# Optimization experiments

Measured on AMD Instinct MI355X. Metric: run time of the kernel, lower is better.

The kernel has to match this reference:

```python
import jax, jax.numpy as jnp
import numpy as np

L = 4          # num layers
NH = 128       # hidden channels per layer
FC = 16        # frame_channel = patch^2 * C
HP = 32        # H / patch
WP = 32        # W / patch
K = 5          # filter_size
B = 8
T_PREV = 10
T_AFTER = 10
T_TOTAL = T_PREV + T_AFTER - 1  # 19 generated frames
FORGET_BIAS = 1.0


def _conv(x, w):
    # x: [B, Cin, H, W], w: [Cout, Cin, kh, kw], stride 1, SAME padding
    return jax.lax.conv_general_dilated(
        x, w, (1, 1), 'SAME', dimension_numbers=('NCHW', 'OIHW', 'NCHW'))


def _st_lstm_cell(x, h, c, m, Wx, Wh, Wm, Wo, Wl):
    # Standard PredRNN SpatioTemporalLSTMCell (bias-free convs, no layer norm)
    xc = _conv(x, Wx)   # [B, 7*NH, H, W]
    hc = _conv(h, Wh)   # [B, 4*NH, H, W]
    mc = _conv(m, Wm)   # [B, 3*NH, H, W]
    i_x, f_x, g_x, i_xp, f_xp, g_xp, o_x = jnp.split(xc, 7, axis=1)
    i_h, f_h, g_h, o_h = jnp.split(hc, 4, axis=1)
    i_m, f_m, g_m = jnp.split(mc, 3, axis=1)

    i_t = jax.nn.sigmoid(i_x + i_h)
    f_t = jax.nn.sigmoid(f_x + f_h + FORGET_BIAS)
    g_t = jnp.tanh(g_x + g_h)
    c_new = f_t * c + i_t * g_t

    i_tp = jax.nn.sigmoid(i_xp + i_m)
    f_tp = jax.nn.sigmoid(f_xp + f_m + FORGET_BIAS)
    g_tp = jnp.tanh(g_xp + g_m)
    m_new = f_tp * m + i_tp * g_tp

    mem = jnp.concatenate([c_new, m_new], axis=1)  # [B, 2*NH, H, W]
    o_t = jax.nn.sigmoid(o_x + o_h + _conv(mem, Wo))
    h_new = o_t * jnp.tanh(_conv(mem, Wl))
    return h_new, c_new, m_new


def setup_inputs() -> dict:
    key = jax.random.key(0)
    ks = jax.random.split(key, 9)
    s = jnp.float32(0.02)  # small init scale to keep gates in a sane range
    return {
        'frames_tensor': jax.random.normal(ks[0], (B, T_PREV + T_AFTER, HP, WP, FC), jnp.float32),
        'mask_true': jax.random.uniform(ks[1], (B, T_AFTER - 1, HP, WP, FC), jnp.float32),
        'Wx0': jax.random.normal(ks[2], (7 * NH, FC, K, K), jnp.float32) * s,
        'Wx': jax.random.normal(ks[3], (L - 1, 7 * NH, NH, K, K), jnp.float32) * s,
        'Wh': jax.random.normal(ks[4], (L, 4 * NH, NH, K, K), jnp.float32) * s,
        'Wm': jax.random.normal(ks[5], (L, 3 * NH, NH, K, K), jnp.float32) * s,
        'Wo': jax.random.normal(ks[6], (L, NH, 2 * NH, K, K), jnp.float32) * s,
        'Wl': jax.random.normal(ks[7], (L, NH, 2 * NH, 1, 1), jnp.float32) * s,
        'Wout': jax.random.normal(ks[8], (FC, NH, 1, 1), jnp.float32) * s,
    }


def reference(frames_tensor, mask_true, Wx0, Wx, Wh, Wm, Wo, Wl, Wout):
    # [B,T,H,W,C] -> [B,T,C,H,W]
    frames = jnp.transpose(frames_tensor, (0, 1, 4, 2, 3))
    mask = jnp.transpose(mask_true, (0, 1, 4, 2, 3))

    # For t < data_previous the input is the ground-truth frame (mask == 1);
    # afterwards it is blended with the previous generation x_gen.
    ones = jnp.ones((B, T_PREV, FC, HP, WP), frames.dtype)
    mask_seq = jnp.concatenate([ones, mask], axis=1)  # [B, T_TOTAL, C, H, W]

    frames_t = jnp.transpose(frames[:, :T_TOTAL], (1, 0, 2, 3, 4))  # [T,B,C,H,W]
    mask_t = jnp.transpose(mask_seq, (1, 0, 2, 3, 4))               # [T,B,C,H,W]

    h0 = jnp.zeros((L, B, NH, HP, WP), frames.dtype)
    c0 = jnp.zeros((L, B, NH, HP, WP), frames.dtype)
    m0 = jnp.zeros((B, NH, HP, WP), frames.dtype)
    xg0 = jnp.zeros((B, FC, HP, WP), frames.dtype)

    def step(carry, xs):
        h, c, m, x_gen = carry
        frame, msk = xs
        net = msk * frame + (1.0 - msk) * x_gen
        h_new, c_new, m = _st_lstm_cell(net, h[0], c[0], m, Wx0, Wh[0], Wm[0], Wo[0], Wl[0])
        hs, cs = [h_new], [c_new]
        for i in range(1, L):
            hi, ci, m = _st_lstm_cell(hs[-1], h[i], c[i], m, Wx[i - 1], Wh[i], Wm[i], Wo[i], Wl[i])
            hs.append(hi)
            cs.append(ci)
        x_gen = _conv(hs[-1], Wout)  # 1x1 conv, no bias
        return (jnp.stack(hs), jnp.stack(cs), m, x_gen), x_gen

    _, next_frames = jax.lax.scan(step, (h0, c0, m0, xg0), (frames_t, mask_t))
    # [T,B,C,H,W] -> [B,T,H,W,C]
    return jnp.transpose(next_frames, (1, 0, 3, 4, 2))
```

## Files before the change

kernel.cpp:

```cpp
#include <hip/hip_runtime.h>
#include <math.h>

#define TT 19
#define TPREV 10

typedef __attribute__((ext_vector_type(8))) short bf8v;
typedef __attribute__((ext_vector_type(4))) float f4v;
typedef __attribute__((ext_vector_type(16))) float f16v;

__device__ __forceinline__ float sigmoidf_(float x){ return 1.f/(1.f+expf(-x)); }
__device__ __forceinline__ unsigned short f2bf(float x){
    unsigned int u = __float_as_uint(x);
    u += 0x7FFFu + ((u>>16)&1u);
    return (unsigned short)(u>>16);
}
__device__ __forceinline__ float bf2f(unsigned short b){ return __uint_as_float(((unsigned int)b)<<16); }

#define GLDS(g, l) __builtin_amdgcn_global_load_lds( \
    (const __attribute__((address_space(1))) void*)(g),   \
    (__attribute__((address_space(3))) void*)(l), 16, 0, 0)

struct HSeg {
    const unsigned short* in;
    int cl;
    int c0;
    int nch;
    int tap0, ntaps, five;
};
struct HJob {
    const unsigned short* wt;
    float* out;
    int cout_stride, pad;
    HSeg s;
};
struct HJobs14 { HJob j[14]; };
struct HJobs9  { HJob j[9]; };


template<typename JOBS>
__global__ __launch_bounds__(256, 2) void hconvA_kernel(JOBS jobs)
{
    __shared__ unsigned short sA[16384];
    __shared__ unsigned short sH[15360];
    const int tid = threadIdx.x;

    const int nb   = gridDim.x * gridDim.y;
    const int per8 = nb >> 3;
    const int bidl = blockIdx.x + gridDim.x * blockIdx.y;
    const int g    = (bidl & 7) * per8 + (bidl >> 3);
    const int jy   = g >> 5;
    const int xt   = g & 31;
    const HJob jb = jobs.j[jy];

    const int ng0 = xt << 8;
    const int bb = ng0 >> 10, p0 = ng0 & 1023;
    const int y0 = p0 >> 5;

    const int lane = tid & 63, wv = tid >> 6;
    const int wm = (wv & 1) << 6;
    const int wn = (wv >> 1) << 7;
    const int col = lane & 31, ll5 = lane >> 5;

    int bofs0[4];
#pragma unroll
    for (int ni = 0; ni < 4; ++ni) {
        const int ln = wn + ni * 32 + col;
        const int cell = ((ln >> 5) + 2) * 40 + (ln & 31) + 4;
        bofs0[ni] = cell * 8 + ll5 * 3840;
    }
    const int rowA0 = (wm + col) * 8;
    const int oA = ll5 * 1024;

    f16v acc[2][4];
#pragma unroll
    for (int i = 0; i < 2; ++i)
#pragma unroll
        for (int j = 0; j < 4; ++j) acc[i][j] = (f16v)0.f;

    const HSeg sg = jb.s;
    const unsigned short* inb = sg.in + ((size_t)bb << (10 + sg.cl));
    const unsigned short* wptr = jb.wt;
    const int ntaps = sg.ntaps;
    const int ntot = sg.nch * ntaps;

    {
        const int c0 = sg.c0;
#pragma unroll
        for (int k = 0; k < 8; ++k) {
            const int s = tid + k * 256;
            if (s < 1920) {
                const int r = s / 160;
                const int rem = s - r * 160;
                const int cc = rem >> 2, G = rem & 3;
                const int y = y0 + r - 2, x = cc - 4;
                const bool okv = ((unsigned)y < 32u) & ((unsigned)x < 32u);
                const int yc = okv ? y : 0, xc = okv ? x : 0;
                bf8v v = *(const bf8v*)(inb + ((((yc << 5) + xc)) << sg.cl) + c0 + G * 8);
                if (!okv) v = (bf8v)(short)0;
                *(bf8v*)&sH[(G * 480 + r * 40 + cc) * 8] = v;
            }
        }
    }
    GLDS(wptr + tid * 8,                &sA[tid * 8]);
    GLDS(wptr + (tid + 256) * 8,        &sA[(tid + 256) * 8]);
    GLDS(wptr + 4096 + tid * 8,         &sA[4096 + tid * 8]);
    GLDS(wptr + 4096 + (tid + 256) * 8, &sA[4096 + (tid + 256) * 8]);
    wptr += 8192;

    int bcur = 0, tc = 0, ch = 0;
    for (int t = 0; t < ntot; ++t) {
        if (tc == ntaps) {
            tc = 0; ++ch;
            __syncthreads();
            const int c0 = sg.c0 + ch * 32;
#pragma unroll
            for (int k = 0; k < 8; ++k) {
                const int s = tid + k * 256;
                if (s < 1920) {
                    const int r = s / 160;
                    const int rem = s - r * 160;
                    const int cc = rem >> 2, G = rem & 3;
                    const int y = y0 + r - 2, x = cc - 4;
                    const bool okv = ((unsigned)y < 32u) & ((unsigned)x < 32u);
                    const int yc = okv ? y : 0, xc = okv ? x : 0;
                    bf8v v = *(const bf8v*)(inb + ((((yc << 5) + xc)) << sg.cl) + c0 + G * 8);
                    if (!okv) v = (bf8v)(short)0;
                    *(bf8v*)&sH[(G * 480 + r * 40 + cc) * 8] = v;
                }
            }
        }
        if (t + 2 < ntot) {
            const int b2 = (bcur + 2) & 3;
            GLDS(wptr + tid * 8,         &sA[b2 * 4096 + tid * 8]);
            GLDS(wptr + (tid + 256) * 8, &sA[b2 * 4096 + (tid + 256) * 8]);
            wptr += 4096;
        }
        int tO = 0;
        if (sg.five) {
            const int tap = sg.tap0 + tc;
            const int t5 = (tap * 52) >> 8;
            tO = ((t5 - 2) * 40 + (tap - t5 * 5 - 2)) * 8;
        }
        if (t + 2 < ntot)      asm volatile("s_waitcnt vmcnt(4) lgkmcnt(0)" ::: "memory");
        else if (t + 1 < ntot) asm volatile("s_waitcnt vmcnt(2) lgkmcnt(0)" ::: "memory");
        else                   asm volatile("s_waitcnt vmcnt(0) lgkmcnt(0)" ::: "memory");
        __builtin_amdgcn_s_barrier();
        __builtin_amdgcn_sched_barrier(0);

        const unsigned short* sAb = &sA[bcur * 4096];
        bf8v av[2][2], bv[2][4];
#pragma unroll
        for (int s = 0; s < 2; ++s) {
#pragma unroll
            for (int mi = 0; mi < 2; ++mi)
                av[s][mi] = *(const bf8v*)&sAb[s * 2048 + oA + rowA0 + mi * 256];
#pragma unroll
            for (int ni = 0; ni < 4; ++ni)
                bv[s][ni] = *(const bf8v*)&sH[bofs0[ni] + tO + s * 7680];
        }
        __builtin_amdgcn_s_setprio(1);
#pragma unroll
        for (int s = 0; s < 2; ++s)
#pragma unroll
            for (int mi = 0; mi < 2; ++mi)
#pragma unroll
                for (int ni = 0; ni < 4; ++ni)
                    acc[mi][ni] = __builtin_amdgcn_mfma_f32_32x32x16_bf16(
                        av[s][mi], bv[s][ni], acc[mi][ni], 0, 0, 0);
        __builtin_amdgcn_s_setprio(0);

        bcur = (bcur + 1) & 3;
        ++tc;
    }

    const int nfix = ng0 + wn + col;
#pragma unroll
    for (int ni = 0; ni < 4; ++ni) {
        const int n = nfix + ni * 32;
        float* ob = jb.out + (size_t)n * jb.cout_stride;
#pragma unroll
        for (int mi = 0; mi < 2; ++mi) {
            const int mb = wm + mi * 32 + 4 * ll5;
            const f16v a = acc[mi][ni];
#pragma unroll
            for (int qd = 0; qd < 4; ++qd) {
                f4v v;
                v[0] = a[qd * 4 + 0]; v[1] = a[qd * 4 + 1];
                v[2] = a[qd * 4 + 2]; v[3] = a[qd * 4 + 3];
                *(f4v*)(ob + mb + qd * 8) = v;
            }
        }
    }
}

template<typename JOBS>
__global__ __launch_bounds__(256) void hconv_kernel(JOBS jobs)
{
    __shared__ unsigned short sA[8192];
    __shared__ unsigned short sH[10240];
    const HJob jb = jobs.j[blockIdx.y];
    const int tid = threadIdx.x;

    const int ng0 = blockIdx.x * 128;
    const int bb = ng0 >> 10, p0 = ng0 & 1023;
    const int y0 = p0 >> 5;

    const int lane = tid & 63, wv = tid >> 6;
    const int wm = (wv & 1) << 6;
    const int wn = (wv >> 1) << 6;
    const int col = lane & 31, ll5 = lane >> 5;

    int bofs0[2];
#pragma unroll
    for (int ni = 0; ni < 2; ++ni) {
        const int ln = wn + ni * 32 + col;
        const int cell = ((ln >> 5) + 2) * 40 + (ln & 31) + 4;
        bofs0[ni] = cell * 8 + ll5 * 2560;
    }

    f16v acc[2][2];
#pragma unroll
    for (int i = 0; i < 2; ++i)
#pragma unroll
        for (int j = 0; j < 2; ++j) acc[i][j] = (f16v)0.f;

    const HSeg sg = jb.s;
    const unsigned short* inb = sg.in + ((size_t)bb << (10 + sg.cl));
    const unsigned short* wptr = jb.wt;
    int buf = 0;
    bool first = true;
    for (int ch = 0; ch < sg.nch; ++ch) {
        const int c0 = sg.c0 + ch * 32;
#pragma unroll
        for (int k = 0; k < 5; ++k) {
            const int s = tid + k * 256;
            const int r = s / 160;
            const int rem = s - r * 160;
            const int cc = rem >> 2, G = rem & 3;
            const int y = y0 + r - 2, x = cc - 4;
            const bool okv = ((unsigned)y < 32u) & ((unsigned)x < 32u);
            const int yc = okv ? y : 0, xc = okv ? x : 0;
            bf8v v = *(const bf8v*)(inb + ((((yc << 5) + xc)) << sg.cl) + c0 + G * 8);
            if (!okv) v = (bf8v)(short)0;
            *(bf8v*)&sH[(G * 320 + r * 40 + cc) * 8] = v;
        }
        if (first) {
            GLDS(wptr + tid * 8,         &sA[tid * 8]);
            GLDS(wptr + (tid + 256) * 8, &sA[(tid + 256) * 8]);
            wptr += 4096;
            first = false;
        }
        __syncthreads();
        for (int t = 0; t < sg.ntaps; ++t) {
            GLDS(wptr + tid * 8,         &sA[(buf ^ 1) * 4096 + tid * 8]);
            GLDS(wptr + (tid + 256) * 8, &sA[(buf ^ 1) * 4096 + (tid + 256) * 8]);
            wptr += 4096;
            int tO = 0;
            if (sg.five) {
                const int tap = sg.tap0 + t;
                const int t5 = (tap * 52) >> 8;
                tO = ((t5 - 2) * 40 + (tap - t5 * 5 - 2)) * 8;
            }
            const unsigned short* sAb = &sA[buf * 4096];
#pragma unroll
            for (int s = 0; s < 2; ++s) {
                const int o = s * 2 + ll5;
                bf8v av[2], bv[2];
#pragma unroll
                for (int mi = 0; mi < 2; ++mi)
                    av[mi] = *(const bf8v*)&sAb[(o * 128 + wm + mi * 32 + col) * 8];
#pragma unroll
                for (int ni = 0; ni < 2; ++ni)
                    bv[ni] = *(const bf8v*)&sH[bofs0[ni] + tO + s * 5120];
#pragma unroll
                for (int mi = 0; mi < 2; ++mi)
#pragma unroll
                    for (int ni = 0; ni < 2; ++ni)
                        acc[mi][ni] = __builtin_amdgcn_mfma_f32_32x32x16_bf16(
                            av[mi], bv[ni], acc[mi][ni], 0, 0, 0);
            }
            __syncthreads();
            buf ^= 1;
        }
    }

    const int nfix = ng0 + wn + col;
#pragma unroll
    for (int ni = 0; ni < 2; ++ni) {
        const int n = nfix + ni * 32;
        float* ob = jb.out + (size_t)n * jb.cout_stride;
#pragma unroll
        for (int mi = 0; mi < 2; ++mi) {
            const int mb = wm + mi * 32 + 4 * ll5;
            const f16v a = acc[mi][ni];
#pragma unroll
            for (int qd = 0; qd < 4; ++qd) {
                f4v v;
                v[0] = a[qd * 4 + 0]; v[1] = a[qd * 4 + 1];
                v[2] = a[qd * 4 + 2]; v[3] = a[qd * 4 + 3];
                *(f4v*)(ob + mb + qd * 8) = v;
            }
        }
    }
}

__global__ __launch_bounds__(256) void packT_kernel(
    const float* __restrict__ src, unsigned short* __restrict__ dst,
    int Cin, int srcTaps, int rowOff, int ci0, int ntaps, int tap0,
    int ciMax, int total)
{
    const int idx = blockIdx.x * 256 + threadIdx.x;
    if (idx >= total) return;
    const int j = idx & 7;
    const int row = (idx >> 3) & 127;
    const int q = (idx >> 10) & 3;
    const int at = idx >> 12;
    const int ch = at / ntaps;
    const int tap = tap0 + (at - ch * ntaps);
    const int ci = ci0 + ch * 32 + q * 8 + j;
    float v = 0.f;
    if (ci < ciMax)
        v = src[((size_t)(rowOff + row) * Cin + ci) * srcTaps + tap];
    dst[idx] = f2bf(v);
}

__global__ __launch_bounds__(256) void net_kernel(
    const float* __restrict__ frames, const float* __restrict__ mask,
    const float* __restrict__ xgen, unsigned short* __restrict__ net, int t)
{
    const int idx = blockIdx.x * 256 + threadIdx.x;
    const int n = idx >> 5, ch = idx & 31;
    float v = 0.f;
    if (ch < 16) {
        const int b = n >> 10, p = n & 1023;
        const float fr = frames[((((size_t)b * 20 + t) << 10) + p) * 16 + ch];
        if (t < TPREV) v = fr;
        else {
            const float mk = mask[((((size_t)b * 9 + (t - TPREV)) << 10) + p) * 16 + ch];
            v = mk * fr + (1.f - mk) * xgen[(size_t)n * 16 + ch];
        }
    }
    net[idx] = f2bf(v);
}

__global__ __launch_bounds__(256) void gates_kernel(
    const float* __restrict__ preA, const float* __restrict__ preB,
    float* __restrict__ c, float* __restrict__ m,
    unsigned short* __restrict__ m_bf, unsigned short* __restrict__ mem)
{
    const int idx = blockIdx.x * 256 + threadIdx.x;
    const int n = idx >> 7, ch = idx & 127;
    const float* pa = preA + (size_t)n * 896 + ch;
    const float* pb = preB + (size_t)n * 896 + ch;
    const float i_ = pa[0]   + pb[0];
    const float f_ = pa[128] + pb[128];
    const float g_ = pa[256] + pb[256];
    const float ip = pa[384] + pb[384];
    const float fp = pa[512] + pb[512];
    const float gp = pa[640] + pb[640];
    const float cn = sigmoidf_(f_ + 1.f) * c[idx] + sigmoidf_(i_) * tanhf(g_);
    const float mn = sigmoidf_(fp + 1.f) * m[idx] + sigmoidf_(ip) * tanhf(gp);
    c[idx] = cn;
    m[idx] = mn;
    m_bf[idx] = f2bf(mn);
    mem[(size_t)n * 256 + ch] = f2bf(cn);
    mem[(size_t)n * 256 + 128 + ch] = f2bf(mn);
}

__global__ __launch_bounds__(256) void hout_kernel(
    const float* __restrict__ preA, const float* __restrict__ preB,
    const float* __restrict__ opart, const float* __restrict__ lconv,
    unsigned short* __restrict__ h)
{
    const int idx = blockIdx.x * 256 + threadIdx.x;
    const int n = idx >> 7, ch = idx & 127;
    float oc = preA[(size_t)n * 896 + 768 + ch] + preB[(size_t)n * 896 + 768 + ch];
#pragma unroll
    for (int j = 0; j < 8; ++j) oc += opart[idx + (size_t)j * 1048576];
    h[idx] = f2bf(sigmoidf_(oc) * tanhf(lconv[idx]));
}

__global__ __launch_bounds__(256) void wout_kernel(
    const unsigned short* __restrict__ h3, const float* __restrict__ wo,
    float* __restrict__ xgen, float* __restrict__ out, int t)
{
    const int idx = blockIdx.x * 256 + threadIdx.x;
    const int n = idx >> 4, ch = idx & 15;
    const int b = n >> 10, p = n & 1023;
    const unsigned short* hr = h3 + (size_t)n * 128;
    const float* wr = wo + ch * 128;
    float acc = 0.f;
#pragma unroll 8
    for (int ci = 0; ci < 128; ++ci)
        acc = fmaf(bf2f(hr[ci]), wr[ci], acc);
    xgen[idx] = acc;
    out[((((size_t)b * TT + t) << 10) + p) * 16 + ch] = acc;
}

extern "C" void kernel_launch(void* const* d_in, const int* in_sizes, int n_in,
                              void* d_out, int out_size, void* d_ws, size_t ws_size,
                              hipStream_t stream)
{
    const float* frames = (const float*)d_in[0];
    const float* mask   = (const float*)d_in[1];
    const float* Wx0    = (const float*)d_in[2];
    const float* Wx     = (const float*)d_in[3];
    const float* Wh     = (const float*)d_in[4];
    const float* Wm     = (const float*)d_in[5];
    const float* Wo     = (const float*)d_in[6];
    const float* Wl     = (const float*)d_in[7];
    const float* Wout   = (const float*)d_in[8];
    float* out = (float*)d_out;

    char* base = (char*)d_ws;
    size_t off = 0;
    auto take = [&](size_t bytes) -> char* {
        char* p = base + off;
        off = (off + bytes + 255) & ~(size_t)255;
        return p;
    };
    float* c0            = (float*)take(4ull * 1048576 * 4);
    float* m32           = (float*)take((size_t)1048576 * 4);
    unsigned short* hbf  = (unsigned short*)take(4ull * 1048576 * 2);
    unsigned short* mbf  = (unsigned short*)take((size_t)1048576 * 2);
    const size_t zbytes = off;
    float* xgen          = (float*)take((size_t)131072 * 4);
    float* preA          = (float*)take((size_t)8192 * 896 * 4);
    float* preB          = (float*)take((size_t)8192 * 896 * 4);
    float* lconv         = (float*)take((size_t)1048576 * 4);
    float* opart         = (float*)take(8ull * 1048576 * 4);
    unsigned short* net  = (unsigned short*)take((size_t)262144 * 2);
    unsigned short* mem  = (unsigned short*)take((size_t)2097152 * 2);
    unsigned short* pa0xT = (unsigned short*)take(((size_t)7 * 25 * 4096 + 4096) * 2);
    unsigned short* paT0 = (unsigned short*)take(((size_t)7 * 100 * 4096 + 4096) * 2);
    unsigned short* paT1 = (unsigned short*)take(((size_t)7 * 200 * 4096 + 4096) * 2);
    unsigned short* paT2 = (unsigned short*)take(((size_t)7 * 200 * 4096 + 4096) * 2);
    unsigned short* paT3 = (unsigned short*)take(((size_t)7 * 200 * 4096 + 4096) * 2);
    unsigned short* paT[4] = { paT0, paT1, paT2, paT3 };
    unsigned short* oT   = (unsigned short*)take((4ull * 200 * 4096 + 4096) * 2);
    unsigned short* lT   = (unsigned short*)take((4ull * 8 * 4096 + 4096) * 2);

    hipMemsetAsync(d_ws, 0, zbytes, stream);

    auto packT = [&](const float* s, unsigned short* d, int Cin, int srcTaps,
                     int rowOff, int ci0, int nch, int ntaps, int tap0, int ciMax) {
        const int total = nch * ntaps * 4096;
        packT_kernel<<<(total + 255) / 256, 256, 0, stream>>>(
            s, d, Cin, srcTaps, rowOff, ci0, ntaps, tap0, ciMax, total);
    };
    const int CIMAXBIG = 1 << 30;
    for (int g = 0; g < 7; ++g) {
        packT(Wx0, pa0xT + (size_t)g * 25 * 4096, 16, 25, g * 128, 0, 1, 25, 0, 16);
        const float* hm0 = (g < 3) ? (Wh + (size_t)g * 128 * 128 * 25)
                         : (g == 6) ? (Wh + (size_t)384 * 128 * 25)
                                    : (Wm + (size_t)(g - 3) * 128 * 128 * 25);
        packT(hm0, paT0 + (size_t)g * 100 * 4096, 128, 25, 0, 0, 4, 25, 0, CIMAXBIG);
        for (int l = 1; l < 4; ++l) {
            packT(Wx + (size_t)(l - 1) * 896 * 128 * 25,
                  paT[l] + (size_t)g * 200 * 4096, 128, 25, g * 128, 0, 4, 25, 0, CIMAXBIG);
            const float* hmsrc = (g < 3) ? (Wh + ((size_t)l * 512 + g * 128) * 128 * 25)
                               : (g == 6) ? (Wh + ((size_t)l * 512 + 384) * 128 * 25)
                                          : (Wm + ((size_t)l * 384 + (g - 3) * 128) * 128 * 25);
            packT(hmsrc, paT[l] + ((size_t)g * 200 + 100) * 4096, 128, 25, 0, 0, 4, 25, 0, CIMAXBIG);
        }
    }
    for (int l = 0; l < 4; ++l) {
        packT(Wo + (size_t)l * 128 * 256 * 25, oT + (size_t)l * 200 * 4096,
              256, 25, 0, 0, 8, 25, 0, CIMAXBIG);
        packT(Wl + (size_t)l * 128 * 256, lT + (size_t)l * 8 * 4096,
              256, 1, 0, 0, 8, 1, 0, CIMAXBIG);
    }

    for (int t = 0; t < TT; ++t) {
        net_kernel<<<1024, 256, 0, stream>>>(frames, mask, xgen, net, t);
        for (int l = 0; l < 4; ++l) {
            unsigned short* hl = hbf + (size_t)l * 1048576;
            HJobs14 JA{};
            if (l == 0) {
                for (int g = 0; g < 7; ++g) {
                    const unsigned short* hmsrc = (g < 3 || g == 6) ? hl : mbf;
                    JA.j[2 * g] = HJob{ pa0xT + (size_t)g * 25 * 4096, preA + g * 128,
                                        896, 0, HSeg{ net, 5, 0, 1, 0, 25, 1 } };
                    JA.j[2 * g + 1] = HJob{ paT0 + (size_t)g * 100 * 4096, preB + g * 128,
                                            896, 0, HSeg{ hmsrc, 7, 0, 4, 0, 25, 1 } };
                }
            } else {
                for (int g = 0; g < 7; ++g) {
                    const unsigned short* hmsrc = (g < 3 || g == 6) ? hl : mbf;
                    JA.j[g] = HJob{ paT[l] + (size_t)g * 200 * 4096, preA + g * 128,
                                    896, 0, HSeg{ hbf + (size_t)(l - 1) * 1048576, 7, 0, 4, 0, 25, 1 } };
                    JA.j[7 + g] = HJob{ paT[l] + ((size_t)g * 200 + 100) * 4096, preB + g * 128,
                                        896, 0, HSeg{ hmsrc, 7, 0, 4, 0, 25, 1 } };
                }
            }
            hconvA_kernel<HJobs14><<<dim3(32, 14), 256, 0, stream>>>(JA);

            gates_kernel<<<4096, 256, 0, stream>>>(preA, preB,
                c0 + (size_t)l * 1048576, m32, mbf, mem);

            HJobs9 JB{};
            for (int jj = 0; jj < 8; ++jj)
                JB.j[jj] = HJob{ oT + ((size_t)l * 200 + jj * 25) * 4096,
                                 opart + (size_t)jj * 1048576, 128, 0,
                                 HSeg{ mem, 8, jj * 32, 1, 0, 25, 1 } };
            JB.j[8] = HJob{ lT + (size_t)l * 8 * 4096, lconv, 128, 0,
                            HSeg{ mem, 8, 0, 8, 0, 1, 0 } };
            hconv_kernel<HJobs9><<<dim3(64, 9), 256, 0, stream>>>(JB);

            hout_kernel<<<4096, 256, 0, stream>>>(preA, preB, opart, lconv, hl);
        }
        wout_kernel<<<512, 256, 0, stream>>>(hbf + (size_t)3 * 1048576, Wout, xgen, out, t);
    }
}
```

Measured before the change: 10.91 ms.

## Process conv taps in pairs per barrier with double-buffered weight pairs

Restructures the hconvA main loop to handle two 5x5 filter taps per barrier step, with weights staged into paired LDS buffers one step ahead. The goal is to halve the number of workgroup barriers and waitcnt stalls per channel chunk and give the MFMA scheduler longer runs of independent work. In exchange, the loop now waits for all outstanding loads (vmcnt(0)) every step, so prefetch depth is shallower. The tap count is also fixed at 25 and the ntaps/five/tap0 fields are ignored, which breaks correctness if any job uses a different tap layout. Halo staging is moved into a helper function.

```diff
diff --git a/kernel.cpp b/kernel.cpp
--- a/kernel.cpp
+++ b/kernel.cpp
@@ -36,6 +36,26 @@
 struct HJobs14 { HJob j[14]; };
 struct HJobs9  { HJob j[9]; };
 
+__device__ __forceinline__ void stage_halo(
+    unsigned short* sH, const unsigned short* inb, int cl, int c0,
+    int y0, int tid)
+{
+#pragma unroll
+    for (int k = 0; k < 8; ++k) {
+        const int s = tid + k * 256;
+        if (s < 1920) {
+            const int r = s / 160;
+            const int rem = s - r * 160;
+            const int cc = rem >> 2, G = rem & 3;
+            const int y = y0 + r - 2, x = cc - 4;
+            const bool okv = ((unsigned)y < 32u) & ((unsigned)x < 32u);
+            const int yc = okv ? y : 0, xc = okv ? x : 0;
+            bf8v v = *(const bf8v*)(inb + ((((yc << 5) + xc)) << cl) + c0 + G * 8);
+            if (!okv) v = (bf8v)(short)0;
+            *(bf8v*)&sH[(G * 480 + r * 40 + cc) * 8] = v;
+        }
+    }
+}
 
 template<typename JOBS>
 __global__ __launch_bounds__(256, 2) void hconvA_kernel(JOBS jobs)
@@ -79,98 +99,86 @@
 
     const HSeg sg = jb.s;
     const unsigned short* inb = sg.in + ((size_t)bb << (10 + sg.cl));
-    const unsigned short* wptr = jb.wt;
-    const int ntaps = sg.ntaps;
-    const int ntot = sg.nch * ntaps;
-
-    {
-        const int c0 = sg.c0;
-#pragma unroll
-        for (int k = 0; k < 8; ++k) {
-            const int s = tid + k * 256;
-            if (s < 1920) {
-                const int r = s / 160;
-                const int rem = s - r * 160;
-                const int cc = rem >> 2, G = rem & 3;
-                const int y = y0 + r - 2, x = cc - 4;
-                const bool okv = ((unsigned)y < 32u) & ((unsigned)x < 32u);
-                const int yc = okv ? y : 0, xc = okv ? x : 0;
-                bf8v v = *(const bf8v*)(inb + ((((yc << 5) + xc)) << sg.cl) + c0 + G * 8);
-                if (!okv) v = (bf8v)(short)0;
-                *(bf8v*)&sH[(G * 480 + r * 40 + cc) * 8] = v;
-            }
-        }
-    }
-    GLDS(wptr + tid * 8,                &sA[tid * 8]);
-    GLDS(wptr + (tid + 256) * 8,        &sA[(tid + 256) * 8]);
-    GLDS(wptr + 4096 + tid * 8,         &sA[4096 + tid * 8]);
-    GLDS(wptr + 4096 + (tid + 256) * 8, &sA[4096 + (tid + 256) * 8]);
-    wptr += 8192;
-
-    int bcur = 0, tc = 0, ch = 0;
-    for (int t = 0; t < ntot; ++t) {
-        if (tc == ntaps) {
-            tc = 0; ++ch;
+    const unsigned short* wissue = jb.wt;
+    const int nch = sg.nch;
+
+    stage_halo(sH, inb, sg.cl, sg.c0, y0, tid);
+    GLDS(wissue + tid * 8,                &sA[tid * 8]);
+    GLDS(wissue + (tid + 256) * 8,        &sA[(tid + 256) * 8]);
+    GLDS(wissue + 4096 + tid * 8,         &sA[4096 + tid * 8]);
+    GLDS(wissue + 4096 + (tid + 256) * 8, &sA[4096 + (tid + 256) * 8]);
+    wissue += 8192;
+
+    int gg = 0;
+    for (int c = 0; c < nch; ++c) {
+        if (c > 0) {
             __syncthreads();
-            const int c0 = sg.c0 + ch * 32;
-#pragma unroll
-            for (int k = 0; k < 8; ++k) {
-                const int s = tid + k * 256;
-                if (s < 1920) {
-                    const int r = s / 160;
-                    const int rem = s - r * 160;
-                    const int cc = rem >> 2, G = rem & 3;
-                    const int y = y0 + r - 2, x = cc - 4;
-                    const bool okv = ((unsigned)y < 32u) & ((unsigned)x < 32u);
-                    const int yc = okv ? y : 0, xc = okv ? x : 0;
-                    bf8v v = *(const bf8v*)(inb + ((((yc << 5) + xc)) << sg.cl) + c0 + G * 8);
-                    if (!okv) v = (bf8v)(short)0;
-                    *(bf8v*)&sH[(G * 480 + r * 40 + cc) * 8] = v;
+            stage_halo(sH, inb, sg.cl, sg.c0 + c * 32, y0, tid);
+        }
+        const bool last = (c == nch - 1);
+        for (int j = 0; j < 13; ++j, ++gg) {
+            asm volatile("s_waitcnt vmcnt(0) lgkmcnt(0)" ::: "memory");
+            __builtin_amdgcn_s_barrier();
+            __builtin_amdgcn_sched_barrier(0);
+            const int nIss = (j == 11) ? 1 : ((j == 12) ? (last ? 0 : 2) : 2);
+            const int sb1 = ((gg + 1) & 1) << 1;
+            for (int q = 0; q < nIss; ++q) {
+                GLDS(wissue + tid * 8,         &sA[(sb1 + q) * 4096 + tid * 8]);
+                GLDS(wissue + (tid + 256) * 8, &sA[(sb1 + q) * 4096 + (tid + 256) * 8]);
+                wissue += 4096;
+            }
+            const int sb0 = (gg & 1) << 1;
+            const int k0 = j << 1;
+            const bool pair = (j < 12);
+            int t5 = (k0 * 52) >> 8;
+            const int tOa = ((t5 - 2) * 40 + (k0 - t5 * 5 - 2)) * 8;
+            const unsigned short* sA0 = &sA[sb0 * 4096];
+            bf8v av0[2][2], bv0[2][4], av1[2][2], bv1[2][4];
+#pragma unroll
+            for (int s = 0; s < 2; ++s) {
+#pragma unroll
+                for (int mi = 0; mi < 2; ++mi)
+                    av0[s][mi] = *(const bf8v*)&sA0[s * 2048 + oA + rowA0 + mi * 256];
+#pragma unroll
+                for (int ni = 0; ni < 4; ++ni)
+                    bv0[s][ni] = *(const bf8v*)&sH[bofs0[ni] + tOa + s * 7680];
+            }
+            if (pair) {
+                const int k1 = k0 + 1;
+                t5 = (k1 * 52) >> 8;
+                const int tOb = ((t5 - 2) * 40 + (k1 - t5 * 5 - 2)) * 8;
+                const unsigned short* sA1 = &sA[(sb0 + 1) * 4096];
+#pragma unroll
+                for (int s = 0; s < 2; ++s) {
+#pragma unroll
+                    for (int mi = 0; mi < 2; ++mi)
+                        av1[s][mi] = *(const bf8v*)&sA1[s * 2048 + oA + rowA0 + mi * 256];
+#pragma unroll
+                    for (int ni = 0; ni < 4; ++ni)
+                        bv1[s][ni] = *(const bf8v*)&sH[bofs0[ni] + tOb + s * 7680];
                 }
             }
-        }
-        if (t + 2 < ntot) {
-            const int b2 = (bcur + 2) & 3;
-            GLDS(wptr + tid * 8,         &sA[b2 * 4096 + tid * 8]);
-            GLDS(wptr + (tid + 256) * 8, &sA[b2 * 4096 + (tid + 256) * 8]);
-            wptr += 4096;
-        }
-        int tO = 0;
-        if (sg.five) {
-            const int tap = sg.tap0 + tc;
-            const int t5 = (tap * 52) >> 8;
-            tO = ((t5 - 2) * 40 + (tap - t5 * 5 - 2)) * 8;
-        }
-        if (t + 2 < ntot)      asm volatile("s_waitcnt vmcnt(4) lgkmcnt(0)" ::: "memory");
-        else if (t + 1 < ntot) asm volatile("s_waitcnt vmcnt(2) lgkmcnt(0)" ::: "memory");
-        else                   asm volatile("s_waitcnt vmcnt(0) lgkmcnt(0)" ::: "memory");
-        __builtin_amdgcn_s_barrier();
-        __builtin_amdgcn_sched_barrier(0);
-
-        const unsigned short* sAb = &sA[bcur * 4096];
-        bf8v av[2][2], bv[2][4];
-#pragma unroll
-        for (int s = 0; s < 2; ++s) {
-#pragma unroll
-            for (int mi = 0; mi < 2; ++mi)
-                av[s][mi] = *(const bf8v*)&sAb[s * 2048 + oA + rowA0 + mi * 256];
-#pragma unroll
-            for (int ni = 0; ni < 4; ++ni)
-                bv[s][ni] = *(const bf8v*)&sH[bofs0[ni] + tO + s * 7680];
-        }
-        __builtin_amdgcn_s_setprio(1);
-#pragma unroll
-        for (int s = 0; s < 2; ++s)
-#pragma unroll
-            for (int mi = 0; mi < 2; ++mi)
-#pragma unroll
-                for (int ni = 0; ni < 4; ++ni)
-                    acc[mi][ni] = __builtin_amdgcn_mfma_f32_32x32x16_bf16(
-                        av[s][mi], bv[s][ni], acc[mi][ni], 0, 0, 0);
-        __builtin_amdgcn_s_setprio(0);
-
-        bcur = (bcur + 1) & 3;
-        ++tc;
+            __builtin_amdgcn_s_setprio(1);
+#pragma unroll
+            for (int s = 0; s < 2; ++s)
+#pragma unroll
+                for (int mi = 0; mi < 2; ++mi)
+#pragma unroll
+                    for (int ni = 0; ni < 4; ++ni)
+                        acc[mi][ni] = __builtin_amdgcn_mfma_f32_32x32x16_bf16(
+                            av0[s][mi], bv0[s][ni], acc[mi][ni], 0, 0, 0);
+            if (pair) {
+#pragma unroll
+                for (int s = 0; s < 2; ++s)
+#pragma unroll
+                    for (int mi = 0; mi < 2; ++mi)
+#pragma unroll
+                        for (int ni = 0; ni < 4; ++ni)
+                            acc[mi][ni] = __builtin_amdgcn_mfma_f32_32x32x16_bf16(
+                                av1[s][mi], bv1[s][ni], acc[mi][ni], 0, 0, 0);
+            }
+            __builtin_amdgcn_s_setprio(0);
+        }
     }
 
     const int nfix = ng0 + wn + col;
```

Measured after the change: 11.01 ms. No clear change (+0.9%).
